# Performance work log

Hardware: AMD Instinct MI355X
Metric: run time of the kernel (lower is better)

The kernel has to match this reference:

```python
import jax, jax.numpy as jnp
import numpy as np

IRREPS = [(32, 0), (16, 1), (8, 2)]          # (multiplicity, l)
DIMS = [m * (2 * l + 1) for m, l in IRREPS]  # [32, 48, 40]
OFF = np.concatenate([[0], np.cumsum(DIMS)]).astype(int)
FEAT = int(OFF[-1])                          # 120
H = 4                                        # num_heads
EPS = 1e-5
N_NODES = 50000
N_EDGES = 800000


def split(x):
    # split last axis into per-irrep blocks [..., mul, 2l+1]
    return [x[..., OFF[i]:OFF[i + 1]].reshape(x.shape[:-1] + (m, 2 * l + 1))
            for i, (m, l) in enumerate(IRREPS)]


def merge(blocks, lead):
    return jnp.concatenate([b.reshape(lead + (-1,)) for b in blocks], axis=-1)


def o3_linear(x, Ws):
    # e3nn o3.Linear: mixes multiplicities within each irrep type, 1/sqrt(fan_in) norm
    bs = split(x)
    out = [jnp.einsum('...im,io->...om', b, W) / np.sqrt(m)
           for b, W, (m, l) in zip(bs, Ws, IRREPS)]
    return merge(out, x.shape[:-1])


def norm_act(x):
    # e3nn nn.NormActivation with sigmoid: y = sigmoid(|x|) * x / |x| per irrep
    out = []
    for b in split(x):
        n = jnp.sqrt(jnp.sum(b * b, axis=-1, keepdims=True) + EPS * EPS)
        out.append(jax.nn.sigmoid(n) * b / n)
    return merge(out, x.shape[:-1])


def tp_dot(q, k, Wd):
    # FullyConnectedTensorProduct(q_ir, k_ir, 'Hx0e'), component normalization:
    # per-edge weighted inner products between matching irreps -> [E, H]
    fan = sum(m * m * (2 * l + 1) for m, l in IRREPS)
    out = 0.0
    for qb, kb, W, (m, l) in zip(split(q), split(k), Wd, IRREPS):
        out = out + jnp.einsum('eim,ejm,ijh->eh', qb, kb, W) / np.sqrt(2 * l + 1)
    return out / np.sqrt(fan)


def setup_inputs() -> dict:
    key = jax.random.key(0)
    ks = jax.random.split(key, 16)
    inp = {"node_features": jax.random.normal(ks[0], (N_NODES, FEAT), jnp.float32)}
    i = 1
    for name in ("Wq", "Wk", "Wv"):
        for j, (m, l) in enumerate(IRREPS):
            inp[f"{name}{j}"] = jax.random.normal(ks[i], (m, m), jnp.float32); i += 1
    for j, (m, l) in enumerate(IRREPS):
        inp[f"Wd{j}"] = jax.random.normal(ks[i], (m, m, H), jnp.float32); i += 1
    inp["edge_dst"] = jax.random.randint(ks[i], (N_EDGES,), 0, N_NODES); i += 1
    inp["edge_src"] = jax.random.randint(ks[i], (N_EDGES,), 0, N_NODES)
    return inp


def reference(node_features, Wq0, Wq1, Wq2, Wk0, Wk1, Wk2, Wv0, Wv1, Wv2,
              Wd0, Wd1, Wd2, edge_dst, edge_src):
    N = node_features.shape[0]
    q = norm_act(o3_linear(node_features, [Wq0, Wq1, Wq2]))              # [N, F]
    k = norm_act(o3_linear(node_features[edge_src], [Wk0, Wk1, Wk2]))    # [E, F]
    v_node = norm_act(o3_linear(node_features, [Wv0, Wv1, Wv2]))         # [N, F]
    v = v_node[edge_src]                                                 # [E, F]
    exp = jnp.exp(tp_dot(q[edge_dst], k, [Wd0, Wd1, Wd2]))               # [E, H]
    exp = jnp.mean(exp, axis=1, keepdims=True)                           # [E, 1]
    z = jax.ops.segment_sum(exp, edge_dst, num_segments=N)               # [N, 1]
    z = jnp.where(z == 0, 1.0, z)
    alpha = exp / z[edge_dst]                                            # [E, 1]
    f_out = jax.ops.segment_sum(jnp.sqrt(jax.nn.relu(alpha)) * v,
                                edge_dst, num_segments=N)                # [N, F]
    return f_out + v_node
```

## Files before the change

### kernel.cpp

```cpp
#include <hip/hip_runtime.h>
#include <math.h>

#define FEAT 120
#define HCNT 4

__device__ __forceinline__ float nact_scale(float sumsq) {
    float n = sqrtf(sumsq + 1e-10f);
    float sig = 1.0f / (1.0f + expf(-n));
    return sig / n;
}

#define INV_S32 0.17677669529663687f
#define INV_S16 0.25f
#define INV_S8  0.35355339059327373f
#define S_IR0 0.02175970668223486f
#define S_IR1 0.012562972567021898f
#define S_IR2 0.009731317442393031f


__global__ __launch_bounds__(256) void zero_int_kernel(int* __restrict__ p, int n) {
    int i = blockIdx.x * 256 + threadIdx.x;
    if (i < n) p[i] = 0;
}

__global__ __launch_bounds__(256) void hist_kernel(const int* __restrict__ dst,
                                                   int* __restrict__ cnt, int E) {
    int e = blockIdx.x * 256 + threadIdx.x;
    if (e < E) atomicAdd(&cnt[dst[e]], 1);
}

__global__ __launch_bounds__(256) void scan_block_kernel(const int* __restrict__ cnt,
                                                         int* __restrict__ excl,
                                                         int* __restrict__ bsum, int n) {
    __shared__ int s[256];
    int t = threadIdx.x;
    int i = blockIdx.x * 256 + t;
    int v = (i < n) ? cnt[i] : 0;
    s[t] = v;
    __syncthreads();
    for (int off = 1; off < 256; off <<= 1) {
        int add = (t >= off) ? s[t - off] : 0;
        __syncthreads();
        s[t] += add;
        __syncthreads();
    }
    if (i < n) excl[i] = s[t] - v;
    if (t == 255) bsum[blockIdx.x] = s[255];
}

__global__ __launch_bounds__(256) void scan_sums_kernel(int* __restrict__ bsum, int nb) {
    __shared__ int s[256];
    int t = threadIdx.x;
    int v = (t < nb) ? bsum[t] : 0;
    s[t] = v;
    __syncthreads();
    for (int off = 1; off < 256; off <<= 1) {
        int add = (t >= off) ? s[t - off] : 0;
        __syncthreads();
        s[t] += add;
        __syncthreads();
    }
    if (t < nb) bsum[t] = s[t] - v;
}

__global__ __launch_bounds__(256) void add_offsets_kernel(int* __restrict__ offsets,
                                                          const int* __restrict__ bsum,
                                                          int* __restrict__ cursor,
                                                          int n, int E) {
    int i = blockIdx.x * 256 + threadIdx.x;
    if (i < n) {
        int off = offsets[i] + bsum[i >> 8];
        offsets[i] = off;
        cursor[i] = off;
    }
    if (i == 0) offsets[n] = E;
}

__global__ __launch_bounds__(256) void scatter_kernel(const int* __restrict__ dst,
                                                      const int* __restrict__ src,
                                                      int* __restrict__ cursor,
                                                      int* __restrict__ ssrc, int E) {
    int e = blockIdx.x * 256 + threadIdx.x;
    if (e < E) {
        int pos = atomicAdd(&cursor[dst[e]], 1);
        ssrc[pos] = src[e];
    }
}


__global__ __launch_bounds__(256) void node_qkv_kernel(
    const float* __restrict__ x,
    const float* __restrict__ Wq0, const float* __restrict__ Wq1, const float* __restrict__ Wq2,
    const float* __restrict__ Wk0, const float* __restrict__ Wk1, const float* __restrict__ Wk2,
    const float* __restrict__ Wv0, const float* __restrict__ Wv1, const float* __restrict__ Wv2,
    float* __restrict__ qnode, float* __restrict__ knode, float* __restrict__ vnode, int N)
{
    __shared__ float sWq0[1024], sWq1[256], sWq2[64];
    __shared__ float sWk0[1024], sWk1[256], sWk2[64];
    __shared__ float sWv0[1024], sWv1[256], sWv2[64];

    int t = threadIdx.x;
    for (int i = t; i < 1024; i += 256) { sWq0[i] = Wq0[i]; sWk0[i] = Wk0[i]; sWv0[i] = Wv0[i]; }
    if (t < 256) { sWq1[t] = Wq1[t]; sWk1[t] = Wk1[t]; sWv1[t] = Wv1[t]; }
    if (t < 64)  { sWq2[t] = Wq2[t]; sWk2[t] = Wk2[t]; sWv2[t] = Wv2[t]; }
    __syncthreads();

    int lane = t & 63, wid = t >> 6;
    int ngrp = (N + 3) >> 2;
    for (int grp = blockIdx.x; grp < ngrp; grp += gridDim.x) {
        int node = __builtin_amdgcn_readfirstlane(grp * 4 + wid);
        if (node >= N) continue;
        const float* xr = x + (size_t)node * FEAT;
        float* qr = qnode + (size_t)node * FEAT;
        float* kr = knode + (size_t)node * FEAT;
        float* vr = vnode + (size_t)node * FEAT;
        if (lane < 32) {
            int o = lane;
            float q = 0, k = 0, v = 0;
            #pragma unroll 8
            for (int i = 0; i < 32; i++) {
                float xi = xr[i];
                q = fmaf(xi, sWq0[i * 32 + o], q);
                k = fmaf(xi, sWk0[i * 32 + o], k);
                v = fmaf(xi, sWv0[i * 32 + o], v);
            }
            q *= INV_S32; k *= INV_S32; v *= INV_S32;
            q *= nact_scale(q * q);
            k *= nact_scale(k * k);
            v *= nact_scale(v * v);
            qr[o] = q; kr[o] = k; vr[o] = v;
        } else if (lane < 48) {
            int o = lane - 32;
            float q[3] = {0,0,0}, k[3] = {0,0,0}, v[3] = {0,0,0};
            for (int i = 0; i < 16; i++) {
                float wq = sWq1[i * 16 + o], wk = sWk1[i * 16 + o], wv = sWv1[i * 16 + o];
                #pragma unroll
                for (int c = 0; c < 3; c++) {
                    float xi = xr[32 + i * 3 + c];
                    q[c] = fmaf(xi, wq, q[c]);
                    k[c] = fmaf(xi, wk, k[c]);
                    v[c] = fmaf(xi, wv, v[c]);
                }
            }
            float nq = 0, nk = 0, nv = 0;
            #pragma unroll
            for (int c = 0; c < 3; c++) {
                q[c] *= INV_S16; k[c] *= INV_S16; v[c] *= INV_S16;
                nq += q[c]*q[c]; nk += k[c]*k[c]; nv += v[c]*v[c];
            }
            float sq = nact_scale(nq), sk = nact_scale(nk), sv = nact_scale(nv);
            #pragma unroll
            for (int c = 0; c < 3; c++) {
                int f = 32 + o * 3 + c;
                qr[f] = q[c]*sq; kr[f] = k[c]*sk; vr[f] = v[c]*sv;
            }
        } else if (lane < 56) {
            int o = lane - 48;
            float q[5] = {0,0,0,0,0}, k[5] = {0,0,0,0,0}, v[5] = {0,0,0,0,0};
            for (int i = 0; i < 8; i++) {
                float wq = sWq2[i * 8 + o], wk = sWk2[i * 8 + o], wv = sWv2[i * 8 + o];
                #pragma unroll
                for (int c = 0; c < 5; c++) {
                    float xi = xr[80 + i * 5 + c];
                    q[c] = fmaf(xi, wq, q[c]);
                    k[c] = fmaf(xi, wk, k[c]);
                    v[c] = fmaf(xi, wv, v[c]);
                }
            }
            float nq = 0, nk = 0, nv = 0;
            #pragma unroll
            for (int c = 0; c < 5; c++) {
                q[c] *= INV_S8; k[c] *= INV_S8; v[c] *= INV_S8;
                nq += q[c]*q[c]; nk += k[c]*k[c]; nv += v[c]*v[c];
            }
            float sq = nact_scale(nq), sk = nact_scale(nk), sv = nact_scale(nv);
            #pragma unroll
            for (int c = 0; c < 5; c++) {
                int f = 80 + o * 5 + c;
                qr[f] = q[c]*sq; kr[f] = k[c]*sk; vr[f] = v[c]*sv;
            }
        }
    }
}


__global__ __launch_bounds__(256) void node_tq_kernel(
    const float* __restrict__ qnode,
    const float* __restrict__ Wd0, const float* __restrict__ Wd1, const float* __restrict__ Wd2,
    float* __restrict__ tq, int N)
{
    __shared__ float4 sWd0[1024];
    __shared__ float4 sWd1[256];
    __shared__ float4 sWd2[64];
    __shared__ float qs[4][FEAT];

    int t = threadIdx.x;
    for (int i = t; i < 1024; i += 256) sWd0[i] = ((const float4*)Wd0)[i];
    if (t < 256) sWd1[t] = ((const float4*)Wd1)[t];
    if (t < 64)  sWd2[t] = ((const float4*)Wd2)[t];
    __syncthreads();

    int lane = t & 63, wid = t >> 6;
    int ngrp = (N + 3) >> 2;
    for (int grp = blockIdx.x; grp < ngrp; grp += gridDim.x) {
        int node = __builtin_amdgcn_readfirstlane(grp * 4 + wid);
        if (node >= N) continue;
        const float* qr = qnode + (size_t)node * FEAT;
        qs[wid][lane] = qr[lane];
        if (lane < FEAT - 64) qs[wid][64 + lane] = qr[64 + lane];
        __builtin_amdgcn_wave_barrier();

        float* tr = tq + (size_t)node * (HCNT * FEAT);
        if (lane < 32) {
            int j = lane;
            float a0 = 0, a1 = 0, a2 = 0, a3 = 0;
            #pragma unroll 8
            for (int i = 0; i < 32; i++) {
                float qi = qs[wid][i];
                float4 w = sWd0[i * 32 + j];
                a0 = fmaf(qi, w.x, a0); a1 = fmaf(qi, w.y, a1);
                a2 = fmaf(qi, w.z, a2); a3 = fmaf(qi, w.w, a3);
            }
            tr[0 * FEAT + j] = a0 * S_IR0;
            tr[1 * FEAT + j] = a1 * S_IR0;
            tr[2 * FEAT + j] = a2 * S_IR0;
            tr[3 * FEAT + j] = a3 * S_IR0;
        } else if (lane < 48) {
            int j = lane - 32;
            float a[4][3] = {};
            for (int i = 0; i < 16; i++) {
                float4 w = sWd1[i * 16 + j];
                #pragma unroll
                for (int c = 0; c < 3; c++) {
                    float qi = qs[wid][32 + i * 3 + c];
                    a[0][c] = fmaf(qi, w.x, a[0][c]);
                    a[1][c] = fmaf(qi, w.y, a[1][c]);
                    a[2][c] = fmaf(qi, w.z, a[2][c]);
                    a[3][c] = fmaf(qi, w.w, a[3][c]);
                }
            }
            #pragma unroll
            for (int h = 0; h < 4; h++)
                #pragma unroll
                for (int c = 0; c < 3; c++)
                    tr[h * FEAT + 32 + j * 3 + c] = a[h][c] * S_IR1;
        } else if (lane < 56) {
            int j = lane - 48;
            float a[4][5] = {};
            for (int i = 0; i < 8; i++) {
                float4 w = sWd2[i * 8 + j];
                #pragma unroll
                for (int c = 0; c < 5; c++) {
                    float qi = qs[wid][80 + i * 5 + c];
                    a[0][c] = fmaf(qi, w.x, a[0][c]);
                    a[1][c] = fmaf(qi, w.y, a[1][c]);
                    a[2][c] = fmaf(qi, w.z, a[2][c]);
                    a[3][c] = fmaf(qi, w.w, a[3][c]);
                }
            }
            #pragma unroll
            for (int h = 0; h < 4; h++)
                #pragma unroll
                for (int c = 0; c < 5; c++)
                    tr[h * FEAT + 80 + j * 5 + c] = a[h][c] * S_IR2;
        }
        __builtin_amdgcn_wave_barrier();
    }
}


__device__ __forceinline__ float head_reduce(const float tA[4], const float tB[4],
                                             float k0, float k1, int lane) {
    float d0 = fmaf(tA[0], k0, tB[0] * k1);
    float d1 = fmaf(tA[1], k0, tB[1] * k1);
    float d2 = fmaf(tA[2], k0, tB[2] * k1);
    float d3 = fmaf(tA[3], k0, tB[3] * k1);
    d0 += __shfl_xor(d0, 16, 64); d0 += __shfl_xor(d0, 32, 64);
    d1 += __shfl_xor(d1, 16, 64); d1 += __shfl_xor(d1, 32, 64);
    d2 += __shfl_xor(d2, 16, 64); d2 += __shfl_xor(d2, 32, 64);
    d3 += __shfl_xor(d3, 16, 64); d3 += __shfl_xor(d3, 32, 64);
    int g = lane >> 4;
    float v = (g == 0) ? d0 : (g == 1) ? d1 : (g == 2) ? d2 : d3;
    v += __shfl_xor(v, 1, 64); v += __shfl_xor(v, 2, 64);
    v += __shfl_xor(v, 4, 64); v += __shfl_xor(v, 8, 64);
    float e = expf(v);
    e += __shfl_xor(e, 16, 64);
    e += __shfl_xor(e, 32, 64);
    return 0.25f * e;
}

__global__ __launch_bounds__(256) void edge_fused_kernel(
    const float* __restrict__ tq, const float* __restrict__ knode,
    const float* __restrict__ vnode,
    const int* __restrict__ offsets, const int* __restrict__ ssrc,
    float* __restrict__ out, int N)
{
    int lane = threadIdx.x & 63, wid = threadIdx.x >> 6;
    int node = blockIdx.x * 4 + wid;
    if (node >= N) return;
    node = __builtin_amdgcn_readfirstlane(node);
    bool hi = lane < (FEAT - 64);

    const float* tr = tq + (size_t)node * (HCNT * FEAT);
    float tA[4], tB[4];
    #pragma unroll
    for (int h = 0; h < 4; h++) {
        tA[h] = tr[h * FEAT + lane];
        tB[h] = hi ? tr[h * FEAT + 64 + lane] : 0.0f;
    }

    int beg = offsets[node], end = offsets[node + 1];
    float zsum = 0.0f, acc0 = 0.0f, acc1 = 0.0f;

    int p = beg;
    for (; p + 4 <= end; p += 4) {
        int s0 = __builtin_amdgcn_readfirstlane(ssrc[p]);
        int s1 = __builtin_amdgcn_readfirstlane(ssrc[p + 1]);
        int s2 = __builtin_amdgcn_readfirstlane(ssrc[p + 2]);
        int s3 = __builtin_amdgcn_readfirstlane(ssrc[p + 3]);
        const float* kr0 = knode + (size_t)s0 * FEAT;
        const float* kr1 = knode + (size_t)s1 * FEAT;
        const float* kr2 = knode + (size_t)s2 * FEAT;
        const float* kr3 = knode + (size_t)s3 * FEAT;
        const float* vr0 = vnode + (size_t)s0 * FEAT;
        const float* vr1 = vnode + (size_t)s1 * FEAT;
        const float* vr2 = vnode + (size_t)s2 * FEAT;
        const float* vr3 = vnode + (size_t)s3 * FEAT;
        float k0a = kr0[lane], k1a = hi ? kr0[64 + lane] : 0.0f;
        float k0b = kr1[lane], k1b = hi ? kr1[64 + lane] : 0.0f;
        float k0c = kr2[lane], k1c = hi ? kr2[64 + lane] : 0.0f;
        float k0d = kr3[lane], k1d = hi ? kr3[64 + lane] : 0.0f;
        float v0a = vr0[lane], v1a = hi ? vr0[64 + lane] : 0.0f;
        float v0b = vr1[lane], v1b = hi ? vr1[64 + lane] : 0.0f;
        float v0c = vr2[lane], v1c = hi ? vr2[64 + lane] : 0.0f;
        float v0d = vr3[lane], v1d = hi ? vr3[64 + lane] : 0.0f;
        float exa = head_reduce(tA, tB, k0a, k1a, lane);
        float exb = head_reduce(tA, tB, k0b, k1b, lane);
        float exc = head_reduce(tA, tB, k0c, k1c, lane);
        float exd = head_reduce(tA, tB, k0d, k1d, lane);
        zsum += (exa + exb) + (exc + exd);
        float wa = sqrtf(exa), wb = sqrtf(exb), wc = sqrtf(exc), wd = sqrtf(exd);
        acc0 = fmaf(wa, v0a, acc0); acc1 = fmaf(wa, v1a, acc1);
        acc0 = fmaf(wb, v0b, acc0); acc1 = fmaf(wb, v1b, acc1);
        acc0 = fmaf(wc, v0c, acc0); acc1 = fmaf(wc, v1c, acc1);
        acc0 = fmaf(wd, v0d, acc0); acc1 = fmaf(wd, v1d, acc1);
    }
    for (; p < end; ++p) {
        int s0 = __builtin_amdgcn_readfirstlane(ssrc[p]);
        const float* kr0 = knode + (size_t)s0 * FEAT;
        const float* vr0 = vnode + (size_t)s0 * FEAT;
        float k0a = kr0[lane], k1a = hi ? kr0[64 + lane] : 0.0f;
        float v0a = vr0[lane], v1a = hi ? vr0[64 + lane] : 0.0f;
        float exa = head_reduce(tA, tB, k0a, k1a, lane);
        zsum += exa;
        float wa = sqrtf(exa);
        acc0 = fmaf(wa, v0a, acc0); acc1 = fmaf(wa, v1a, acc1);
    }

    float scale = (zsum > 0.0f) ? rsqrtf(zsum) : 0.0f;
    const float* vself = vnode + (size_t)node * FEAT;
    float* orow = out + (size_t)node * FEAT;
    orow[lane] = vself[lane] + acc0 * scale;
    if (hi) orow[64 + lane] = vself[64 + lane] + acc1 * scale;
}


extern "C" void kernel_launch(void* const* d_in, const int* in_sizes, int n_in,
                              void* d_out, int out_size, void* d_ws, size_t ws_size,
                              hipStream_t stream) {
    const float* x   = (const float*)d_in[0];
    const float* Wq0 = (const float*)d_in[1];
    const float* Wq1 = (const float*)d_in[2];
    const float* Wq2 = (const float*)d_in[3];
    const float* Wk0 = (const float*)d_in[4];
    const float* Wk1 = (const float*)d_in[5];
    const float* Wk2 = (const float*)d_in[6];
    const float* Wv0 = (const float*)d_in[7];
    const float* Wv1 = (const float*)d_in[8];
    const float* Wv2 = (const float*)d_in[9];
    const float* Wd0 = (const float*)d_in[10];
    const float* Wd1 = (const float*)d_in[11];
    const float* Wd2 = (const float*)d_in[12];
    const int* edge_dst = (const int*)d_in[13];
    const int* edge_src = (const int*)d_in[14];
    float* out = (float*)d_out;

    int N = in_sizes[0] / FEAT;
    int E = in_sizes[13];

    float* ws = (float*)d_ws;
    float* qnode = ws;
    float* knode = qnode + (size_t)N * FEAT;
    float* vnode = knode + (size_t)N * FEAT;
    float* tq    = vnode + (size_t)N * FEAT;
    int* offsets = (int*)(tq + (size_t)N * HCNT * FEAT);
    int* cursor  = offsets + (N + 1);
    int* bsum    = cursor + N;
    int* ssrc    = bsum + 256;

    int NB = (N + 255) / 256;
    int EB = (E + 255) / 256;
    int NW = (N + 3) / 4;

    zero_int_kernel<<<NB, 256, 0, stream>>>(cursor, N);
    hist_kernel<<<EB, 256, 0, stream>>>(edge_dst, cursor, E);
    scan_block_kernel<<<NB, 256, 0, stream>>>(cursor, offsets, bsum, N);
    scan_sums_kernel<<<1, 256, 0, stream>>>(bsum, NB);
    add_offsets_kernel<<<NB, 256, 0, stream>>>(offsets, bsum, cursor, N, E);
    scatter_kernel<<<EB, 256, 0, stream>>>(edge_dst, edge_src, cursor, ssrc, E);

    node_qkv_kernel<<<2048, 256, 0, stream>>>(x, Wq0, Wq1, Wq2, Wk0, Wk1, Wk2,
                                              Wv0, Wv1, Wv2, qnode, knode, vnode, N);
    node_tq_kernel<<<2048, 256, 0, stream>>>(qnode, Wd0, Wd1, Wd2, tq, N);
    edge_fused_kernel<<<NW, 256, 0, stream>>>(tq, knode, vnode, offsets, ssrc, out, N);
}
```

Before: 458.2 us.

## Store k/v/tq in bf16 and compute edge attention scores with MFMA

Stores k, v and the per-node q·Wd tensor in bf16, padded to 128 columns, which halves the gather traffic in the edge pass. The edge kernel now scores 16 neighbour edges at once with 16x16x32 bf16 MFMA instructions instead of cross-lane shuffle reductions. It then accumulates packed bf16 v rows with shuffled weights. The self term v_node is written into the output by the node kernel and the edge kernel adds to it. This trades precision (bf16 k, v and tq) for less memory bandwidth and fewer ALU/shuffle instructions.

```diff
diff --git a/kernel.cpp b/kernel.cpp
--- a/kernel.cpp
+++ b/kernel.cpp
@@ -3,11 +3,22 @@
 
 #define FEAT 120
 #define HCNT 4
+
+typedef unsigned short ushort_t;
+typedef unsigned int uint_t;
+typedef __attribute__((ext_vector_type(8))) short short8;
+typedef __attribute__((ext_vector_type(4))) float floatx4;
 
 __device__ __forceinline__ float nact_scale(float sumsq) {
     float n = sqrtf(sumsq + 1e-10f);
     float sig = 1.0f / (1.0f + expf(-n));
     return sig / n;
+}
+
+__device__ __forceinline__ ushort_t bf16r(float f) {
+    uint_t u = __float_as_uint(f);
+    u += 0x7fff + ((u >> 16) & 1);
+    return (ushort_t)(u >> 16);
 }
 
 #define INV_S32 0.17677669529663687f
@@ -93,7 +104,8 @@
     const float* __restrict__ Wq0, const float* __restrict__ Wq1, const float* __restrict__ Wq2,
     const float* __restrict__ Wk0, const float* __restrict__ Wk1, const float* __restrict__ Wk2,
     const float* __restrict__ Wv0, const float* __restrict__ Wv1, const float* __restrict__ Wv2,
-    float* __restrict__ qnode, float* __restrict__ knode, float* __restrict__ vnode, int N)
+    float* __restrict__ qnode, ushort_t* __restrict__ kb, ushort_t* __restrict__ vb,
+    float* __restrict__ out, int N)
 {
     __shared__ float sWq0[1024], sWq1[256], sWq2[64];
     __shared__ float sWk0[1024], sWk1[256], sWk2[64];
@@ -112,8 +124,9 @@
         if (node >= N) continue;
         const float* xr = x + (size_t)node * FEAT;
         float* qr = qnode + (size_t)node * FEAT;
-        float* kr = knode + (size_t)node * FEAT;
-        float* vr = vnode + (size_t)node * FEAT;
+        ushort_t* kr = kb + (size_t)node * 128;
+        ushort_t* vr = vb + (size_t)node * 128;
+        float* orow = out + (size_t)node * FEAT;
         if (lane < 32) {
             int o = lane;
             float q = 0, k = 0, v = 0;
@@ -128,7 +141,7 @@
             q *= nact_scale(q * q);
             k *= nact_scale(k * k);
             v *= nact_scale(v * v);
-            qr[o] = q; kr[o] = k; vr[o] = v;
+            qr[o] = q; kr[o] = bf16r(k); vr[o] = bf16r(v); orow[o] = v;
         } else if (lane < 48) {
             int o = lane - 32;
             float q[3] = {0,0,0}, k[3] = {0,0,0}, v[3] = {0,0,0};
@@ -152,7 +165,8 @@
             #pragma unroll
             for (int c = 0; c < 3; c++) {
                 int f = 32 + o * 3 + c;
-                qr[f] = q[c]*sq; kr[f] = k[c]*sk; vr[f] = v[c]*sv;
+                float vv = v[c]*sv;
+                qr[f] = q[c]*sq; kr[f] = bf16r(k[c]*sk); vr[f] = bf16r(vv); orow[f] = vv;
             }
         } else if (lane < 56) {
             int o = lane - 48;
@@ -177,8 +191,12 @@
             #pragma unroll
             for (int c = 0; c < 5; c++) {
                 int f = 80 + o * 5 + c;
-                qr[f] = q[c]*sq; kr[f] = k[c]*sk; vr[f] = v[c]*sv;
-            }
+                float vv = v[c]*sv;
+                qr[f] = q[c]*sq; kr[f] = bf16r(k[c]*sk); vr[f] = bf16r(vv); orow[f] = vv;
+            }
+        } else {
+            int p = 120 + (lane - 56);
+            kr[p] = 0; vr[p] = 0;
         }
     }
 }
@@ -187,7 +205,7 @@
 __global__ __launch_bounds__(256) void node_tq_kernel(
     const float* __restrict__ qnode,
     const float* __restrict__ Wd0, const float* __restrict__ Wd1, const float* __restrict__ Wd2,
-    float* __restrict__ tq, int N)
+    ushort_t* __restrict__ tqb, int N)
 {
     __shared__ float4 sWd0[1024];
     __shared__ float4 sWd1[256];
@@ -210,7 +228,7 @@
         if (lane < FEAT - 64) qs[wid][64 + lane] = qr[64 + lane];
         __builtin_amdgcn_wave_barrier();
 
-        float* tr = tq + (size_t)node * (HCNT * FEAT);
+        ushort_t* tr = tqb + (size_t)node * 512;
         if (lane < 32) {
             int j = lane;
             float a0 = 0, a1 = 0, a2 = 0, a3 = 0;
@@ -221,10 +239,10 @@
                 a0 = fmaf(qi, w.x, a0); a1 = fmaf(qi, w.y, a1);
                 a2 = fmaf(qi, w.z, a2); a3 = fmaf(qi, w.w, a3);
             }
-            tr[0 * FEAT + j] = a0 * S_IR0;
-            tr[1 * FEAT + j] = a1 * S_IR0;
-            tr[2 * FEAT + j] = a2 * S_IR0;
-            tr[3 * FEAT + j] = a3 * S_IR0;
+            tr[0 * 128 + j] = bf16r(a0 * S_IR0);
+            tr[1 * 128 + j] = bf16r(a1 * S_IR0);
+            tr[2 * 128 + j] = bf16r(a2 * S_IR0);
+            tr[3 * 128 + j] = bf16r(a3 * S_IR0);
         } else if (lane < 48) {
             int j = lane - 32;
             float a[4][3] = {};
@@ -243,7 +261,7 @@
             for (int h = 0; h < 4; h++)
                 #pragma unroll
                 for (int c = 0; c < 3; c++)
-                    tr[h * FEAT + 32 + j * 3 + c] = a[h][c] * S_IR1;
+                    tr[h * 128 + 32 + j * 3 + c] = bf16r(a[h][c] * S_IR1);
         } else if (lane < 56) {
             int j = lane - 48;
             float a[4][5] = {};
@@ -262,36 +280,20 @@
             for (int h = 0; h < 4; h++)
                 #pragma unroll
                 for (int c = 0; c < 5; c++)
-                    tr[h * FEAT + 80 + j * 5 + c] = a[h][c] * S_IR2;
+                    tr[h * 128 + 80 + j * 5 + c] = bf16r(a[h][c] * S_IR2);
+        } else {
+            int r = lane - 56;
+            #pragma unroll
+            for (int h = 0; h < 4; h++) tr[h * 128 + 120 + r] = 0;
         }
         __builtin_amdgcn_wave_barrier();
     }
 }
 
 
-__device__ __forceinline__ float head_reduce(const float tA[4], const float tB[4],
-                                             float k0, float k1, int lane) {
-    float d0 = fmaf(tA[0], k0, tB[0] * k1);
-    float d1 = fmaf(tA[1], k0, tB[1] * k1);
-    float d2 = fmaf(tA[2], k0, tB[2] * k1);
-    float d3 = fmaf(tA[3], k0, tB[3] * k1);
-    d0 += __shfl_xor(d0, 16, 64); d0 += __shfl_xor(d0, 32, 64);
-    d1 += __shfl_xor(d1, 16, 64); d1 += __shfl_xor(d1, 32, 64);
-    d2 += __shfl_xor(d2, 16, 64); d2 += __shfl_xor(d2, 32, 64);
-    d3 += __shfl_xor(d3, 16, 64); d3 += __shfl_xor(d3, 32, 64);
-    int g = lane >> 4;
-    float v = (g == 0) ? d0 : (g == 1) ? d1 : (g == 2) ? d2 : d3;
-    v += __shfl_xor(v, 1, 64); v += __shfl_xor(v, 2, 64);
-    v += __shfl_xor(v, 4, 64); v += __shfl_xor(v, 8, 64);
-    float e = expf(v);
-    e += __shfl_xor(e, 16, 64);
-    e += __shfl_xor(e, 32, 64);
-    return 0.25f * e;
-}
-
-__global__ __launch_bounds__(256) void edge_fused_kernel(
-    const float* __restrict__ tq, const float* __restrict__ knode,
-    const float* __restrict__ vnode,
+__global__ __launch_bounds__(256) void edge_mfma_kernel(
+    const ushort_t* __restrict__ tqb, const ushort_t* __restrict__ kb,
+    const ushort_t* __restrict__ vb,
     const int* __restrict__ offsets, const int* __restrict__ ssrc,
     float* __restrict__ out, int N)
 {
@@ -299,69 +301,83 @@
     int node = blockIdx.x * 4 + wid;
     if (node >= N) return;
     node = __builtin_amdgcn_readfirstlane(node);
-    bool hi = lane < (FEAT - 64);
-
-    const float* tr = tq + (size_t)node * (HCNT * FEAT);
-    float tA[4], tB[4];
-    #pragma unroll
-    for (int h = 0; h < 4; h++) {
-        tA[h] = tr[h * FEAT + lane];
-        tB[h] = hi ? tr[h * FEAT + 64 + lane] : 0.0f;
+    int m = lane & 15, quad = lane >> 4;
+
+    short8 afr[4];
+    if (m < HCNT) {
+        const short8* ap = (const short8*)(tqb + (size_t)node * 512 + m * 128 + quad * 8);
+        #pragma unroll
+        for (int b = 0; b < 4; b++) afr[b] = ap[b * 4];
+    } else {
+        #pragma unroll
+        for (int b = 0; b < 4; b++) afr[b] = (short8){0,0,0,0,0,0,0,0};
     }
 
     int beg = offsets[node], end = offsets[node + 1];
-    float zsum = 0.0f, acc0 = 0.0f, acc1 = 0.0f;
-
-    int p = beg;
-    for (; p + 4 <= end; p += 4) {
-        int s0 = __builtin_amdgcn_readfirstlane(ssrc[p]);
-        int s1 = __builtin_amdgcn_readfirstlane(ssrc[p + 1]);
-        int s2 = __builtin_amdgcn_readfirstlane(ssrc[p + 2]);
-        int s3 = __builtin_amdgcn_readfirstlane(ssrc[p + 3]);
-        const float* kr0 = knode + (size_t)s0 * FEAT;
-        const float* kr1 = knode + (size_t)s1 * FEAT;
-        const float* kr2 = knode + (size_t)s2 * FEAT;
-        const float* kr3 = knode + (size_t)s3 * FEAT;
-        const float* vr0 = vnode + (size_t)s0 * FEAT;
-        const float* vr1 = vnode + (size_t)s1 * FEAT;
-        const float* vr2 = vnode + (size_t)s2 * FEAT;
-        const float* vr3 = vnode + (size_t)s3 * FEAT;
-        float k0a = kr0[lane], k1a = hi ? kr0[64 + lane] : 0.0f;
-        float k0b = kr1[lane], k1b = hi ? kr1[64 + lane] : 0.0f;
-        float k0c = kr2[lane], k1c = hi ? kr2[64 + lane] : 0.0f;
-        float k0d = kr3[lane], k1d = hi ? kr3[64 + lane] : 0.0f;
-        float v0a = vr0[lane], v1a = hi ? vr0[64 + lane] : 0.0f;
-        float v0b = vr1[lane], v1b = hi ? vr1[64 + lane] : 0.0f;
-        float v0c = vr2[lane], v1c = hi ? vr2[64 + lane] : 0.0f;
-        float v0d = vr3[lane], v1d = hi ? vr3[64 + lane] : 0.0f;
-        float exa = head_reduce(tA, tB, k0a, k1a, lane);
-        float exb = head_reduce(tA, tB, k0b, k1b, lane);
-        float exc = head_reduce(tA, tB, k0c, k1c, lane);
-        float exd = head_reduce(tA, tB, k0d, k1d, lane);
-        zsum += (exa + exb) + (exc + exd);
-        float wa = sqrtf(exa), wb = sqrtf(exb), wc = sqrtf(exc), wd = sqrtf(exd);
-        acc0 = fmaf(wa, v0a, acc0); acc1 = fmaf(wa, v1a, acc1);
-        acc0 = fmaf(wb, v0b, acc0); acc1 = fmaf(wb, v1b, acc1);
-        acc0 = fmaf(wc, v0c, acc0); acc1 = fmaf(wc, v1c, acc1);
-        acc0 = fmaf(wd, v0d, acc0); acc1 = fmaf(wd, v1d, acc1);
-    }
-    for (; p < end; ++p) {
-        int s0 = __builtin_amdgcn_readfirstlane(ssrc[p]);
-        const float* kr0 = knode + (size_t)s0 * FEAT;
-        const float* vr0 = vnode + (size_t)s0 * FEAT;
-        float k0a = kr0[lane], k1a = hi ? kr0[64 + lane] : 0.0f;
-        float v0a = vr0[lane], v1a = hi ? vr0[64 + lane] : 0.0f;
-        float exa = head_reduce(tA, tB, k0a, k1a, lane);
-        zsum += exa;
-        float wa = sqrtf(exa);
-        acc0 = fmaf(wa, v0a, acc0); acc1 = fmaf(wa, v1a, acc1);
-    }
-
+    float zpart = 0.0f, accx = 0.0f, accy = 0.0f;
+    const uint_t* vrow = (const uint_t*)vb;
+
+    for (int tb = beg; tb < end; tb += 16) {
+        int rem = end - tb; if (rem > 16) rem = 16;
+        int idx = tb + (m < rem ? m : rem - 1);
+        int src = ssrc[idx];
+        const short8* bp = (const short8*)(kb + (size_t)src * 128 + quad * 8);
+        short8 b0 = bp[0], b1 = bp[4], b2 = bp[8], b3 = bp[12];
+        floatx4 C = {0.0f, 0.0f, 0.0f, 0.0f};
+        C = __builtin_amdgcn_mfma_f32_16x16x32_bf16(afr[0], b0, C, 0, 0, 0);
+        C = __builtin_amdgcn_mfma_f32_16x16x32_bf16(afr[1], b1, C, 0, 0, 0);
+        C = __builtin_amdgcn_mfma_f32_16x16x32_bf16(afr[2], b2, C, 0, 0, 0);
+        C = __builtin_amdgcn_mfma_f32_16x16x32_bf16(afr[3], b3, C, 0, 0, 0);
+
+        float w = 0.0f;
+        if (quad == 0 && m < rem) {
+            float ex = 0.25f * (__expf(C[0]) + __expf(C[1]) + __expf(C[2]) + __expf(C[3]));
+            zpart += ex;
+            w = sqrtf(ex);
+        }
+
+        if (rem == 16) {
+            #pragma unroll
+            for (int e0 = 0; e0 < 16; e0 += 8) {
+                float we[8]; int se[8]; uint_t vp[8];
+                #pragma unroll
+                for (int j = 0; j < 8; j++) {
+                    we[j] = __shfl(w, e0 + j, 64);
+                    se[j] = __shfl(src, e0 + j, 64);
+                }
+                #pragma unroll
+                for (int j = 0; j < 8; j++) vp[j] = vrow[(size_t)se[j] * 64 + lane];
+                #pragma unroll
+                for (int j = 0; j < 8; j++) {
+                    accx = fmaf(we[j], __uint_as_float(vp[j] << 16), accx);
+                    accy = fmaf(we[j], __uint_as_float(vp[j] & 0xffff0000u), accy);
+                }
+            }
+        } else {
+            for (int e = 0; e < rem; e++) {
+                float we = __shfl(w, e, 64);
+                int   se = __shfl(src, e, 64);
+                uint_t vp = vrow[(size_t)se * 64 + lane];
+                accx = fmaf(we, __uint_as_float(vp << 16), accx);
+                accy = fmaf(we, __uint_as_float(vp & 0xffff0000u), accy);
+            }
+        }
+    }
+
+    zpart += __shfl_xor(zpart, 1, 64);
+    zpart += __shfl_xor(zpart, 2, 64);
+    zpart += __shfl_xor(zpart, 4, 64);
+    zpart += __shfl_xor(zpart, 8, 64);
+    float zsum = __shfl(zpart, 0, 64);
     float scale = (zsum > 0.0f) ? rsqrtf(zsum) : 0.0f;
-    const float* vself = vnode + (size_t)node * FEAT;
-    float* orow = out + (size_t)node * FEAT;
-    orow[lane] = vself[lane] + acc0 * scale;
-    if (hi) orow[64 + lane] = vself[64 + lane] + acc1 * scale;
+
+    if (lane < 60) {
+        float2* op = (float2*)(out + (size_t)node * FEAT) + lane;
+        float2 o = *op;
+        o.x = fmaf(accx, scale, o.x);
+        o.y = fmaf(accy, scale, o.y);
+        *op = o;
+    }
 }
 
 
@@ -390,10 +406,10 @@
 
     float* ws = (float*)d_ws;
     float* qnode = ws;
-    float* knode = qnode + (size_t)N * FEAT;
-    float* vnode = knode + (size_t)N * FEAT;
-    float* tq    = vnode + (size_t)N * FEAT;
-    int* offsets = (int*)(tq + (size_t)N * HCNT * FEAT);
+    ushort_t* kb  = (ushort_t*)(qnode + (size_t)N * FEAT);
+    ushort_t* vb  = kb + (size_t)N * 128;
+    ushort_t* tqb = vb + (size_t)N * 128;
+    int* offsets = (int*)(tqb + (size_t)N * 512);
     int* cursor  = offsets + (N + 1);
     int* bsum    = cursor + N;
     int* ssrc    = bsum + 256;
@@ -410,7 +426,7 @@
     scatter_kernel<<<EB, 256, 0, stream>>>(edge_dst, edge_src, cursor, ssrc, E);
 
     node_qkv_kernel<<<2048, 256, 0, stream>>>(x, Wq0, Wq1, Wq2, Wk0, Wk1, Wk2,
-                                              Wv0, Wv1, Wv2, qnode, knode, vnode, N);
-    node_tq_kernel<<<2048, 256, 0, stream>>>(qnode, Wd0, Wd1, Wd2, tq, N);
-    edge_fused_kernel<<<NW, 256, 0, stream>>>(tq, knode, vnode, offsets, ssrc, out, N);
-}
+                                              Wv0, Wv1, Wv2, qnode, kb, vb, out, N);
+    node_tq_kernel<<<2048, 256, 0, stream>>>(qnode, Wd0, Wd1, Wd2, tqb, N);
+    edge_mfma_kernel<<<NW, 256, 0, stream>>>(tqb, kb, vb, offsets, ssrc, out, N);
+}
```

New measurement: 398.7 us. -13.0%, faster.
